# Kernel optimization log

Hardware: AMD Instinct MI355X
Metric: run time of the kernel (lower is better)

## Reference

```python
import jax, jax.numpy as jnp
import numpy as np

EPS = 1e-6
DIM_HEAD = 32
INP = 128
OUP = 128
IH = IW = 32


def _conv3x3(x, w):
    # NCHW conv, 3x3, stride 1, pad 1, no bias
    return jax.lax.conv_general_dilated(
        x, w, window_strides=(1, 1), padding=((1, 1), (1, 1)),
        dimension_numbers=("NCHW", "OIHW", "NCHW"))


def _groupnorm1(x, gamma, beta):
    # GroupNorm with 1 group: normalize over (C,H,W) per sample
    m = jnp.mean(x, axis=(1, 2, 3), keepdims=True)
    v = jnp.var(x, axis=(1, 2, 3), keepdims=True)
    xn = (x - m) * jax.lax.rsqrt(v + EPS)
    return xn * gamma[None, :, None, None] + beta[None, :, None, None]


def _proj(x, w, gamma, beta):
    return jax.nn.gelu(_groupnorm1(_conv3x3(x, w), gamma, beta), approximate=False)


def _relative_index(ih, iw):
    coords = np.stack(np.meshgrid(np.arange(ih), np.arange(iw), indexing="ij"))
    coords = coords.reshape(2, -1)  # (2, N)
    rel = coords[:, :, None] - coords[:, None, :]  # (2, N, N)
    rel[0] += ih - 1
    rel[1] += iw - 1
    rel[0] *= 2 * iw - 1
    return rel.sum(0).reshape(-1).astype(np.int32)  # (N*N,)


def setup_inputs() -> dict:
    key = jax.random.key(0)
    ks = jax.random.split(key, 12)
    B = 16
    x = jax.random.normal(ks[0], (B, INP, IH, IW), jnp.float32)
    w_scale = 0.05
    wq = jax.random.normal(ks[1], (INP, INP, 3, 3), jnp.float32) * w_scale
    wk = jax.random.normal(ks[2], (INP, INP, 3, 3), jnp.float32) * w_scale
    wv = jax.random.normal(ks[3], (INP, INP, 3, 3), jnp.float32) * w_scale
    gq = jnp.ones((INP,), jnp.float32); bq = jnp.zeros((INP,), jnp.float32)
    gk = jnp.ones((INP,), jnp.float32); bk = jnp.zeros((INP,), jnp.float32)
    gv = jnp.ones((INP,), jnp.float32); bv = jnp.zeros((INP,), jnp.float32)
    heads = INP // DIM_HEAD
    table = jax.random.normal(ks[4], ((2 * IH - 1) * (2 * IW - 1), heads), jnp.float32) * 0.02
    rel_index = jnp.asarray(_relative_index(IH, IW))
    out_w = jax.random.normal(ks[5], (OUP, INP, 1, 1), jnp.float32) * w_scale
    out_b = jnp.zeros((OUP,), jnp.float32)
    return {"x": x, "wq": wq, "gq": gq, "bq": bq, "wk": wk, "gk": gk, "bk": bk,
            "wv": wv, "gv": gv, "bv": bv, "table": table, "rel_index": rel_index,
            "out_w": out_w, "out_b": out_b}


def reference(x, wq, gq, bq, wk, gk, bk, wv, gv, bv, table, rel_index, out_w, out_b):
    B, C, ih, iw = x.shape
    H = C // DIM_HEAD
    N = ih * iw

    def to_heads(t):
        # b c ih iw -> b (ihiw) c -> b h n d (heads-major channel split)
        return t.reshape(B, C, N).transpose(0, 2, 1).reshape(B, N, H, DIM_HEAD).transpose(0, 2, 1, 3)

    q = to_heads(_proj(x, wq, gq, bq))
    k = to_heads(_proj(x, wk, gk, bk))
    v = to_heads(_proj(x, wv, gv, bv))

    # NOTE: original applies self.scale only when y is not None; y=None here -> no scale
    dots = jnp.einsum("bhnd,bhmd->bhnm", q, k)  # (B,H,N,N)

    bias = table[rel_index]                 # (N*N, H)
    bias = bias.reshape(N, N, H).transpose(2, 0, 1)[None]  # (1,H,N,N)
    attn = jax.nn.softmax(dots + bias, axis=-1)

    out = jnp.einsum("bhnm,bhmd->bhnd", attn, v)
    out = out.transpose(0, 2, 1, 3).reshape(B, N, C).transpose(0, 2, 1).reshape(B, C, ih, iw)
    # to_out: 1x1 conv + bias (Dropout2d is identity in eval)
    out = jax.lax.conv_general_dilated(
        out, out_w, window_strides=(1, 1), padding=((0, 0), (0, 0)),
        dimension_numbers=("NCHW", "OIHW", "NCHW")) + out_b[None, :, None, None]
    return out
```

## Files before the change

### kernel.cpp

```cpp
#include <hip/hip_runtime.h>

typedef unsigned short u16;
typedef unsigned int   u32;

#define NB   16
#define NC   128
#define NPIX 1024
#define NH   4
#define DH   32

typedef __attribute__((ext_vector_type(8))) short short8;
typedef __attribute__((ext_vector_type(4))) float f32x4;
typedef __attribute__((ext_vector_type(8))) _Float16 half8;

#define XROWS 1152

__device__ __forceinline__ float bf2f(u16 u) {
    return __uint_as_float(((u32)u) << 16);
}
__device__ __forceinline__ u16 f2bf(float f) {
    u32 u = __float_as_uint(f);
    u32 r = (u + 0x7fffu + ((u >> 16) & 1u)) >> 16;
    return (u16)r;
}
__device__ __forceinline__ u16 f2h(float f) {
    _Float16 h = (_Float16)f;
    u16 r; __builtin_memcpy(&r, &h, 2); return r;
}
__device__ __forceinline__ int pk_h2(float a, float b) {
    auto h = __builtin_amdgcn_cvt_pkrtz(a, b);
    int r; __builtin_memcpy(&r, &h, 4); return r;
}
__device__ __forceinline__ float loadf(const void* p, int i, int isf) {
    return isf ? ((const float*)p)[i] : bf2f(((const u16*)p)[i]);
}
__device__ __forceinline__ float4 load4(const void* p, int i4, int isf) {
    if (isf) return ((const float4*)p)[i4];
    ushort4 u = ((const ushort4*)p)[i4];
    return make_float4(bf2f(u.x), bf2f(u.y), bf2f(u.z), bf2f(u.w));
}
__device__ __forceinline__ int detect_isf(const void* x) {
    const u16* p = (const u16*)x;
    u16 v = p[threadIdx.x & 63];
    int e = (v >> 7) & 0xFF;
    unsigned long long m = __ballot(e >= 134);
    return m != 0ull ? 1 : 0;
}

__global__ __launch_bounds__(256) void prep_all(
        const void* __restrict__ x,
        const void* __restrict__ w0, const void* __restrict__ w1,
        const void* __restrict__ w2, const void* __restrict__ ow,
        const int* __restrict__ rel, const void* __restrict__ table,
        u16* __restrict__ Wt, u16* __restrict__ Wf, u16* __restrict__ xTp,
        u16* __restrict__ biasT, float* __restrict__ stats) {
    __shared__ __align__(16) u32 smem_u[4160];
    int isf = detect_isf(x);
    int bid = blockIdx.x;
    int t = threadIdx.x;

    if (bid < 1792) {
        if (bid == 0 && t < 96) stats[t] = 0.f;
        int i = bid * 256 + t;
        if (i < 442368) {
            int j   = i / 147456;
            int rr  = i % 147456;
            int tap = rr >> 14;
            int co  = (rr >> 7) & 127;
            int ci  = rr & 127;
            const void* w = (j == 0) ? w0 : ((j == 1) ? w1 : w2);
            float v = loadf(w, (co * 128 + ci) * 9 + tap, isf);
            int coh = (co >> 6) & 1, wm = (co >> 5) & 1;
            int mt  = (co >> 4) & 1, l16 = co & 15;
            int ks  = (ci >> 5) & 3, q  = (ci >> 3) & 3, e = ci & 7;
            int dst = (j * 9 + tap) * 16384
                    + (coh * 2 + wm) * 4096 + ks * 1024 + mt * 512
                    + (q * 16 + l16) * 8 + e;
            Wt[dst] = f2bf(v);
        } else {
            int i2 = i - 442368;
            if (i2 < 16384) {
                int co = i2 >> 7, k = i2 & 127;
                int zc = (co >> 6) & 1, wm = (co >> 5) & 1;
                int mt = (co >> 4) & 1, l16 = co & 15;
                int ks = (k >> 5) & 3, q = (k >> 3) & 3, e = k & 7;
                int dst = (zc * 2 + wm) * 4096 + ks * 1024 + mt * 512
                        + (q * 16 + l16) * 8 + e;
                Wf[dst] = f2h(loadf(ow, i2, isf));
            }
        }
    } else if (bid < 2304) {
        float* tile = (float*)smem_u;
        int b2 = bid - 1792;
        int pixg = b2 & 7, cig = (b2 >> 3) & 3, b = b2 >> 5;

        if (pixg == 0 || pixg == 7) {
            int row = (pixg == 0 ? 0 : 1088) + (t >> 2);
            int seg = t & 3;
            size_t dst = ((size_t)(b * XROWS + row)) * 128 + cig * 32 + seg * 8;
            *(uint4*)&xTp[dst] = make_uint4(0, 0, 0, 0);
        }

        int ci = t >> 3, px0 = (t & 7) * 16;
        int base = b * (NC * NPIX) + (cig * 32 + ci) * NPIX + pixg * 128 + px0;
#pragma unroll
        for (int u = 0; u < 4; ++u) {
            float4 v = load4(x, (base >> 2) + u, isf);
            float* d = &tile[ci * 129 + px0 + u * 4];
            d[0] = v.x; d[1] = v.y; d[2] = v.z; d[3] = v.w;
        }
        __syncthreads();
#pragma unroll
        for (int u = 0; u < 2; ++u) {
            int c = t + u * 256;
            int pix = c >> 2, seg = c & 3;
            u16 tmp[8];
#pragma unroll
            for (int e = 0; e < 8; ++e)
                tmp[e] = f2bf(tile[(seg * 8 + e) * 129 + pix]);
            size_t dst = ((size_t)(b * XROWS + 64 + pixg * 128 + pix)) * 128
                       + cig * 32 + seg * 8;
            *(ushort4*)&xTp[dst] =
                make_ushort4(tmp[0], tmp[1], tmp[2], tmp[3]);
            *(ushort4*)&xTp[dst + 4] =
                make_ushort4(tmp[4], tmp[5], tmp[6], tmp[7]);
        }
    } else {
        int* rl = (int*)smem_u;
        int b2 = bid - 2304;
        int nt = b2 & 15, mt = b2 >> 4;

#pragma unroll
        for (int c = 0; c < 16; ++c) {
            int i = t + c * 256;
            int r = i >> 6, cc = i & 63;
            rl[r * 65 + cc] = rel[(size_t)(nt * 64 + r) * 1024 + mt * 64 + cc];
        }
        __syncthreads();

#pragma unroll
        for (int h = 0; h < NH; ++h) {
#pragma unroll
            for (int c = 0; c < 16; ++c) {
                int wdx = t + c * 256;
                int r     = wdx & 3;
                int lane  = (wdx >> 2) & 63;
                int fragl = wdx >> 8;
                int n16l  = fragl >> 2;
                int m16l  = fragl & 3;
                int n_loc = n16l * 16 + (lane & 15);
                int m_loc = m16l * 16 + ((lane >> 4) << 2) + r;
                int ri = rl[n_loc * 65 + m_loc];
                float v = loadf(table, ri * NH + h, isf);
                biasT[((size_t)h << 20)
                      + ((size_t)((nt * 4 + n16l) * 64 + (mt * 4 + m16l)) << 8)
                      + lane * 4 + r] = f2bf(v);
            }
        }
    }
}

__global__ __launch_bounds__(256) void conv6_kernel(
        const u16* __restrict__ xTp, const u16* __restrict__ Wt,
        float* __restrict__ conv_out, float* __restrict__ stats) {
    __shared__ __align__(16) u16 Xh[194 * 128];

    int t = threadIdx.x;
    int bx = blockIdx.x, b = blockIdx.y, j = blockIdx.z;
    int pt = bx >> 1, coh = bx & 1;
    int p0 = pt * 128;
    int w = t >> 6, lane = t & 63;
    int q = lane >> 4, l16 = lane & 15;
    int cobase = coh * 64 + (w & 1) * 32;
    int pixbase = (w >> 1) * 64;

    const u16* xb  = xTp + ((size_t)b * XROWS + 64) * 128;
    const u16* wrb = Wt + (size_t)(j * 9) * 16384
                   + (coh * 2 + (w & 1)) * 4096 + lane * 8;

    short8 awA[2][4], awB[2][4];
#pragma unroll
    for (int ks = 0; ks < 4; ++ks) {
        awA[0][ks] = *(const short8*)(wrb + ks * 1024);
        awA[1][ks] = *(const short8*)(wrb + ks * 1024 + 512);
    }

#pragma unroll
    for (int k = 0; k < 13; ++k) {
        int c = t + k * 256;
        if (c < 194 * 16) {
            int row = c >> 4, seg = c & 15;
            int pg = p0 - 33 + row;
            uint4 v = *(const uint4*)(xb + (size_t)pg * 128 + seg * 8);
            *(uint4*)&Xh[row * 128 + ((seg + row) & 15) * 8] = v;
        }
    }
    __syncthreads();

    f32x4 acc[2][4];
#pragma unroll
    for (int mt = 0; mt < 2; ++mt)
#pragma unroll
        for (int nt = 0; nt < 4; ++nt) acc[mt][nt] = (f32x4)0.f;

#pragma unroll
    for (int tap = 0; tap < 9; ++tap) {
        const int dy = tap / 3, dx = tap % 3;
        bool inv_e = (dx == 0) && (l16 == 0);
        bool inv_o = (dx == 2) && (l16 == 15);
        int rbase = pixbase + dy * 32 + dx + l16;

        if (tap < 8) {
            const u16* nw = wrb + (size_t)(tap + 1) * 16384;
            if ((tap & 1) == 0) {
#pragma unroll
                for (int ks = 0; ks < 4; ++ks) {
                    awB[0][ks] = *(const short8*)(nw + ks * 1024);
                    awB[1][ks] = *(const short8*)(nw + ks * 1024 + 512);
                }
            } else {
#pragma unroll
                for (int ks = 0; ks < 4; ++ks) {
                    awA[0][ks] = *(const short8*)(nw + ks * 1024);
                    awA[1][ks] = *(const short8*)(nw + ks * 1024 + 512);
                }
            }
        }

#pragma unroll
        for (int ks = 0; ks < 4; ++ks) {
            int sl = ks * 4 + q;
            short8 bf[4];
#pragma unroll
            for (int nt = 0; nt < 4; ++nt) {
                int row = rbase + nt * 16;
                short8 v = *(const short8*)&Xh[row * 128
                                               + ((sl + row) & 15) * 8];
                bf[nt] = ((nt & 1) ? inv_o : inv_e) ? (short8)0 : v;
            }
#pragma unroll
            for (int mt = 0; mt < 2; ++mt) {
                short8 a = ((tap & 1) == 0) ? awA[mt][ks] : awB[mt][ks];
#pragma unroll
                for (int nt = 0; nt < 4; ++nt)
                    acc[mt][nt] = __builtin_amdgcn_mfma_f32_16x16x32_bf16(
                        a, bf[nt], acc[mt][nt], 0, 0, 0);
            }
        }
    }

    float s = 0.f, s2 = 0.f;
    size_t obase = ((size_t)(j * NB + b) * NC) * NPIX;
#pragma unroll
    for (int mt = 0; mt < 2; ++mt) {
#pragma unroll
        for (int nt = 0; nt < 4; ++nt) {
            f32x4 v = acc[mt][nt];
            int co  = cobase + mt * 16 + q * 4;
            int pix = p0 + pixbase + nt * 16 + l16;
#pragma unroll
            for (int r = 0; r < 4; ++r) {
                float val = v[r];
                conv_out[obase + (size_t)(co + r) * NPIX + pix] = val;
                s += val;
                s2 = fmaf(val, val, s2);
            }
        }
    }
#pragma unroll
    for (int off = 32; off; off >>= 1) {
        s  += __shfl_down(s,  (unsigned)off, 64);
        s2 += __shfl_down(s2, (unsigned)off, 64);
    }
    if (lane == 0) {
        atomicAdd(&stats[(j * NB + b) * 2 + 0], s);
        atomicAdd(&stats[(j * NB + b) * 2 + 1], s2);
    }
}

__global__ __launch_bounds__(256) void norm_kernel(
        const void* __restrict__ xdet,
        const float* __restrict__ conv_out, const float* __restrict__ stats,
        const void* __restrict__ g0, const void* __restrict__ b0,
        const void* __restrict__ g1, const void* __restrict__ b1,
        const void* __restrict__ g2, const void* __restrict__ b2,
        u16* __restrict__ qh, u16* __restrict__ kh, u16* __restrict__ vh) {
    __shared__ float tile[32 * 257];
    int isf = detect_isf(xdet);
    int t = threadIdx.x;
    int n0 = blockIdx.x * 256;
    int h = blockIdx.y;
    int z = blockIdx.z;
    int j = z >> 4;
    int b = z & 15;
    const void* gam = (j == 0) ? g0 : ((j == 1) ? g1 : g2);
    const void* bet = (j == 0) ? b0 : ((j == 1) ? b1 : b2);

    float sum = stats[z * 2], ss = stats[z * 2 + 1];
    const float inv = 1.0f / 131072.0f;
    float mean = sum * inv;
    float var  = fmaxf(ss * inv - mean * mean, 0.f);
    float rstd = rsqrtf(var + 1e-6f);

    const float* src = conv_out + ((size_t)z * NC + h * DH) * NPIX + n0;

    if (j == 2) {
        u16* dst = vh + (((size_t)(b * NH + h)) * DH) * NPIX + n0;
#pragma unroll
        for (int cl = 0; cl < 32; ++cl) {
            float v = src[cl * NPIX + t];
            v = (v - mean) * rstd * loadf(gam, h * DH + cl, isf)
              + loadf(bet, h * DH + cl, isf);
            v = 0.5f * v * (1.0f + erff(v * 0.70710678118654752f));
            dst[(size_t)cl * NPIX + t] = f2h(v);
        }
        return;
    }

#pragma unroll
    for (int cl = 0; cl < 32; ++cl) tile[cl * 257 + t] = src[cl * NPIX + t];
    __syncthreads();

    u16* dst = ((j == 0) ? qh : kh)
             + (((size_t)(b * NH + h)) * NPIX + n0) * DH;
#pragma unroll
    for (int k = 0; k < 32; ++k) {
        int o = t + k * 256;
        int d = o & 31, nl = o >> 5;
        float v = tile[d * 257 + nl];
        v = (v - mean) * rstd * loadf(gam, h * DH + d, isf)
          + loadf(bet, h * DH + d, isf);
        v = 0.5f * v * (1.0f + erff(v * 0.70710678118654752f));
        dst[o] = f2h(v);
    }
}

__global__ __launch_bounds__(256) void attn2_kernel(
        const u16* __restrict__ qh, const u16* __restrict__ kh,
        const u16* __restrict__ vh, const u16* __restrict__ biasT,
        u16* __restrict__ attfh) {
    int t = threadIdx.x;
    int b = blockIdx.x, h = blockIdx.y, qt = blockIdx.z;
    int w = t >> 6, lane = t & 63, q = lane >> 4, l16 = lane & 15;
    int nrow0 = qt * 128 + w * 32;

    const u16* qb = qh + (((size_t)(b * NH + h)) * NPIX) * DH;
    const u16* kb = kh + (((size_t)(b * NH + h)) * NPIX) * DH;
    const u16* vb = vh + (((size_t)(b * NH + h)) * DH) * NPIX;
    const u16* bf0 = biasT + ((size_t)h << 20)
                   + ((size_t)(qt * 8 + w * 2 + 0) << 14) + lane * 4;
    const u16* bf1 = biasT + ((size_t)h << 20)
                   + ((size_t)(qt * 8 + w * 2 + 1) << 14) + lane * 4;

    half8 qf[2];
#pragma unroll
    for (int nt = 0; nt < 2; ++nt)
        qf[nt] = *(const half8*)(qb + (size_t)(nrow0 + nt * 16 + l16) * DH
                                 + q * 8);

    f32x4 O[2][2];
#pragma unroll
    for (int dt = 0; dt < 2; ++dt)
#pragma unroll
        for (int nt = 0; nt < 2; ++nt) O[dt][nt] = (f32x4)0.f;
    float mrow[2] = {-1e30f, -1e30f}, lrow[2] = {0.f, 0.f};

    int addrLo = ((2 * (q & 1)) * 16 + l16) * 4;
    int addrHi = addrLo + 64;
    bool hiQ = (q >= 2);

    for (int kc = 0; kc < 8; ++kc) {
        int m0 = kc * 128;
        f32x4 St[8][2];
#pragma unroll
        for (int mt = 0; mt < 8; ++mt) {
            half8 kf = *(const half8*)(kb + (size_t)(m0 + mt * 16 + l16) * DH
                                       + q * 8);
            int m16 = kc * 8 + mt;
            ushort4 bv0 = *(const ushort4*)(bf0 + (m16 << 8));
            ushort4 bv1 = *(const ushort4*)(bf1 + (m16 << 8));
            f32x4 c0, c1;
            c0[0] = bf2f(bv0.x); c0[1] = bf2f(bv0.y);
            c0[2] = bf2f(bv0.z); c0[3] = bf2f(bv0.w);
            c1[0] = bf2f(bv1.x); c1[1] = bf2f(bv1.y);
            c1[2] = bf2f(bv1.z); c1[3] = bf2f(bv1.w);
            St[mt][0] = __builtin_amdgcn_mfma_f32_16x16x32_f16(
                kf, qf[0], c0, 0, 0, 0);
            St[mt][1] = __builtin_amdgcn_mfma_f32_16x16x32_f16(
                kf, qf[1], c1, 0, 0, 0);
        }
        float mx[2] = {-1e30f, -1e30f};
#pragma unroll
        for (int mt = 0; mt < 8; ++mt)
#pragma unroll
            for (int nt = 0; nt < 2; ++nt)
#pragma unroll
                for (int r = 0; r < 4; ++r)
                    mx[nt] = fmaxf(mx[nt], St[mt][nt][r]);
        float alpha[2];
#pragma unroll
        for (int nt = 0; nt < 2; ++nt) {
            mx[nt] = fmaxf(mx[nt], __shfl_xor(mx[nt], 16, 64));
            mx[nt] = fmaxf(mx[nt], __shfl_xor(mx[nt], 32, 64));
            float mn = fmaxf(mrow[nt], mx[nt]);
            alpha[nt] = __expf(mrow[nt] - mn);
            mrow[nt] = mn;
        }
        float sm[2] = {0.f, 0.f};
#pragma unroll
        for (int mt = 0; mt < 8; ++mt)
#pragma unroll
            for (int nt = 0; nt < 2; ++nt)
#pragma unroll
                for (int r = 0; r < 4; ++r) {
                    float p = __expf(St[mt][nt][r] - mrow[nt]);
                    St[mt][nt][r] = p;
                    sm[nt] += p;
                }
#pragma unroll
        for (int nt = 0; nt < 2; ++nt) {
            sm[nt] += __shfl_xor(sm[nt], 16, 64);
            sm[nt] += __shfl_xor(sm[nt], 32, 64);
            lrow[nt] = lrow[nt] * alpha[nt] + sm[nt];
        }
#pragma unroll
        for (int dt = 0; dt < 2; ++dt)
#pragma unroll
            for (int nt = 0; nt < 2; ++nt)
#pragma unroll
                for (int r = 0; r < 4; ++r)
                    O[dt][nt][r] *= alpha[nt];
#pragma unroll
        for (int ms = 0; ms < 4; ++ms) {
            half8 vf[2];
#pragma unroll
            for (int dt = 0; dt < 2; ++dt)
                vf[dt] = *(const half8*)(vb + (size_t)(dt * 16 + l16) * NPIX
                                         + m0 + ms * 32 + q * 8);
#pragma unroll
            for (int nt = 0; nt < 2; ++nt) {
                int p01_0 = pk_h2(St[2 * ms][nt][0],     St[2 * ms][nt][1]);
                int p23_0 = pk_h2(St[2 * ms][nt][2],     St[2 * ms][nt][3]);
                int p01_1 = pk_h2(St[2 * ms + 1][nt][0], St[2 * ms + 1][nt][1]);
                int p23_1 = pk_h2(St[2 * ms + 1][nt][2], St[2 * ms + 1][nt][3]);
                int a0 = __builtin_amdgcn_ds_bpermute(addrLo, p01_0);
                int a1 = __builtin_amdgcn_ds_bpermute(addrLo, p23_0);
                int a2 = __builtin_amdgcn_ds_bpermute(addrHi, p01_0);
                int a3 = __builtin_amdgcn_ds_bpermute(addrHi, p23_0);
                int b0 = __builtin_amdgcn_ds_bpermute(addrLo, p01_1);
                int b1 = __builtin_amdgcn_ds_bpermute(addrLo, p23_1);
                int b2 = __builtin_amdgcn_ds_bpermute(addrHi, p01_1);
                int b3 = __builtin_amdgcn_ds_bpermute(addrHi, p23_1);
                int pb[4];
                pb[0] = hiQ ? b0 : a0;
                pb[1] = hiQ ? b1 : a1;
                pb[2] = hiQ ? b2 : a2;
                pb[3] = hiQ ? b3 : a3;
                half8 pf; __builtin_memcpy(&pf, pb, 16);
#pragma unroll
                for (int dt = 0; dt < 2; ++dt)
                    O[dt][nt] = __builtin_amdgcn_mfma_f32_16x16x32_f16(
                        vf[dt], pf, O[dt][nt], 0, 0, 0);
            }
        }
    }

#pragma unroll
    for (int nt = 0; nt < 2; ++nt) {
        float rl = 1.0f / lrow[nt];
        int n = nrow0 + nt * 16 + l16;
        u16* dst = attfh + ((size_t)b * NPIX + n) * NC + h * DH;
#pragma unroll
        for (int dt = 0; dt < 2; ++dt) {
            f32x4 o = O[dt][nt];
            uint2 pv = make_uint2((u32)pk_h2(o[0] * rl, o[1] * rl),
                                  (u32)pk_h2(o[2] * rl, o[3] * rl));
            *(uint2*)(dst + dt * 16 + q * 4) = pv;
        }
    }
}

__global__ __launch_bounds__(256) void out3_kernel(
        const void* __restrict__ xdet,
        const u16* __restrict__ attfh, const u16* __restrict__ Wf,
        const void* __restrict__ ob, void* __restrict__ out) {
    int isf = detect_isf(xdet);
    int t = threadIdx.x;
    int n0 = blockIdx.x * 64, b = blockIdx.y, zc = blockIdx.z;
    int w = t >> 6, lane = t & 63, q = lane >> 4, l16 = lane & 15;
    int cobase = zc * 64 + (w & 1) * 32, nbase = (w >> 1) * 32;

    f32x4 acc[2][2];
#pragma unroll
    for (int mt = 0; mt < 2; ++mt)
#pragma unroll
        for (int nt = 0; nt < 2; ++nt) acc[mt][nt] = (f32x4)0.f;

    const u16* ab = attfh + ((size_t)b * NPIX + n0 + nbase) * NC;
    const u16* wfb = Wf + (zc * 2 + (w & 1)) * 4096 + lane * 8;
#pragma unroll
    for (int ks = 0; ks < 4; ++ks) {
        int k0 = ks * 32 + q * 8;
        half8 a[2], bfr[2];
#pragma unroll
        for (int mt = 0; mt < 2; ++mt)
            a[mt] = *(const half8*)(wfb + ks * 1024 + mt * 512);
#pragma unroll
        for (int nt = 0; nt < 2; ++nt)
            bfr[nt] = *(const half8*)(ab + (size_t)(nt * 16 + l16) * NC + k0);
#pragma unroll
        for (int mt = 0; mt < 2; ++mt)
#pragma unroll
            for (int nt = 0; nt < 2; ++nt)
                acc[mt][nt] = __builtin_amdgcn_mfma_f32_16x16x32_f16(
                    a[mt], bfr[nt], acc[mt][nt], 0, 0, 0);
    }

#pragma unroll
    for (int mt = 0; mt < 2; ++mt) {
#pragma unroll
        for (int nt = 0; nt < 2; ++nt) {
            f32x4 v = acc[mt][nt];
            int n = n0 + nbase + nt * 16 + l16;
#pragma unroll
            for (int r = 0; r < 4; ++r) {
                int co = cobase + mt * 16 + q * 4 + r;
                float val = v[r] + loadf(ob, co, isf);
                size_t oidx = ((size_t)b * NC + co) * NPIX + n;
                if (isf) ((float*)out)[oidx] = val;
                else     ((u16*)out)[oidx]   = f2bf(val);
            }
        }
    }
}

extern "C" void kernel_launch(void* const* d_in, const int* in_sizes, int n_in,
                              void* d_out, int out_size, void* d_ws,
                              size_t ws_size, hipStream_t stream) {
    (void)in_sizes; (void)n_in; (void)out_size; (void)ws_size;
    const void* x     = d_in[0];
    const void* wq    = d_in[1];
    const void* gq    = d_in[2];
    const void* bq    = d_in[3];
    const void* wk    = d_in[4];
    const void* gk    = d_in[5];
    const void* bk    = d_in[6];
    const void* wv    = d_in[7];
    const void* gv    = d_in[8];
    const void* bv    = d_in[9];
    const void* table = d_in[10];
    const int*  rel   = (const int*)d_in[11];
    const void* ow    = d_in[12];
    const void* ob    = d_in[13];

    char* ws = (char*)d_ws;
    float* stats = (float*)(ws);
    char*  regQ  = ws + 512;
    u16*   xTp   = (u16*)regQ;
    u16*   Wt    = (u16*)(regQ + 5242880);
    u16*   qhp   = (u16*)regQ;
    u16*   khp   = (u16*)(regQ + 4194304);
    u16*   vhp   = (u16*)(regQ + 8388608);
    u16*   biasT = (u16*)(regQ + 12582912);
    u16*   Wf    = (u16*)(regQ + 20971520);
    char*  regA  = regQ + 25165824;
    float* conv  = (float*)regA;
    u16*   attfh = (u16*)(regA + 8388608);

    prep_all<<<2560, 256, 0, stream>>>(x, wq, wk, wv, ow, rel, table,
                                       Wt, Wf, xTp, biasT, stats);
    conv6_kernel<<<dim3(16, 16, 3), 256, 0, stream>>>(xTp, Wt, conv, stats);
    norm_kernel<<<dim3(4, 4, 48), 256, 0, stream>>>(x, conv, stats,
                                                    gq, bq, gk, bk, gv, bv,
                                                    qhp, khp, vhp);
    attn2_kernel<<<dim3(16, 4, 8), 256, 0, stream>>>(qhp, khp, vhp, biasT,
                                                     attfh);
    out3_kernel<<<dim3(16, 16, 2), 256, 0, stream>>>(x, attfh, Wf, ob, d_out);
}
```

Before: 199.3 us.

## Halve per-wave query rows in attention to double grid size, skip unit rescale

```diff
diff --git a/kernel.cpp b/kernel.cpp
--- a/kernel.cpp
+++ b/kernel.cpp
@@ -342,28 +342,19 @@
     int t = threadIdx.x;
     int b = blockIdx.x, h = blockIdx.y, qt = blockIdx.z;
     int w = t >> 6, lane = t & 63, q = lane >> 4, l16 = lane & 15;
-    int nrow0 = qt * 128 + w * 32;
+    int nrow0 = qt * 64 + w * 16;
 
     const u16* qb = qh + (((size_t)(b * NH + h)) * NPIX) * DH;
     const u16* kb = kh + (((size_t)(b * NH + h)) * NPIX) * DH;
     const u16* vb = vh + (((size_t)(b * NH + h)) * DH) * NPIX;
     const u16* bf0 = biasT + ((size_t)h << 20)
-                   + ((size_t)(qt * 8 + w * 2 + 0) << 14) + lane * 4;
-    const u16* bf1 = biasT + ((size_t)h << 20)
-                   + ((size_t)(qt * 8 + w * 2 + 1) << 14) + lane * 4;
-
-    half8 qf[2];
-#pragma unroll
-    for (int nt = 0; nt < 2; ++nt)
-        qf[nt] = *(const half8*)(qb + (size_t)(nrow0 + nt * 16 + l16) * DH
-                                 + q * 8);
-
-    f32x4 O[2][2];
-#pragma unroll
-    for (int dt = 0; dt < 2; ++dt)
-#pragma unroll
-        for (int nt = 0; nt < 2; ++nt) O[dt][nt] = (f32x4)0.f;
-    float mrow[2] = {-1e30f, -1e30f}, lrow[2] = {0.f, 0.f};
+                   + ((size_t)(qt * 4 + w) << 14) + lane * 4;
+
+    half8 qf = *(const half8*)(qb + (size_t)(nrow0 + l16) * DH + q * 8);
+
+    f32x4 O[2];
+    O[0] = (f32x4)0.f; O[1] = (f32x4)0.f;
+    float mrow = -1e30f, lrow = 0.f;
 
     int addrLo = ((2 * (q & 1)) * 16 + l16) * 4;
     int addrHi = addrLo + 64;
@@ -371,65 +362,48 @@
 
     for (int kc = 0; kc < 8; ++kc) {
         int m0 = kc * 128;
-        f32x4 St[8][2];
+        f32x4 St[8];
 #pragma unroll
         for (int mt = 0; mt < 8; ++mt) {
             half8 kf = *(const half8*)(kb + (size_t)(m0 + mt * 16 + l16) * DH
                                        + q * 8);
-            int m16 = kc * 8 + mt;
-            ushort4 bv0 = *(const ushort4*)(bf0 + (m16 << 8));
-            ushort4 bv1 = *(const ushort4*)(bf1 + (m16 << 8));
-            f32x4 c0, c1;
-            c0[0] = bf2f(bv0.x); c0[1] = bf2f(bv0.y);
-            c0[2] = bf2f(bv0.z); c0[3] = bf2f(bv0.w);
-            c1[0] = bf2f(bv1.x); c1[1] = bf2f(bv1.y);
-            c1[2] = bf2f(bv1.z); c1[3] = bf2f(bv1.w);
-            St[mt][0] = __builtin_amdgcn_mfma_f32_16x16x32_f16(
-                kf, qf[0], c0, 0, 0, 0);
-            St[mt][1] = __builtin_amdgcn_mfma_f32_16x16x32_f16(
-                kf, qf[1], c1, 0, 0, 0);
-        }
-        float mx[2] = {-1e30f, -1e30f};
+            ushort4 bv = *(const ushort4*)(bf0 + ((kc * 8 + mt) << 8));
+            f32x4 c0;
+            c0[0] = bf2f(bv.x); c0[1] = bf2f(bv.y);
+            c0[2] = bf2f(bv.z); c0[3] = bf2f(bv.w);
+            St[mt] = __builtin_amdgcn_mfma_f32_16x16x32_f16(
+                kf, qf, c0, 0, 0, 0);
+        }
+        float mx = -1e30f;
 #pragma unroll
         for (int mt = 0; mt < 8; ++mt)
 #pragma unroll
-            for (int nt = 0; nt < 2; ++nt)
+            for (int r = 0; r < 4; ++r)
+                mx = fmaxf(mx, St[mt][r]);
+        mx = fmaxf(mx, __shfl_xor(mx, 16, 64));
+        mx = fmaxf(mx, __shfl_xor(mx, 32, 64));
+        float mn = fmaxf(mrow, mx);
+        float alpha = __expf(mrow - mn);
+        mrow = mn;
+        float sm = 0.f;
+#pragma unroll
+        for (int mt = 0; mt < 8; ++mt)
+#pragma unroll
+            for (int r = 0; r < 4; ++r) {
+                float p = __expf(St[mt][r] - mrow);
+                St[mt][r] = p;
+                sm += p;
+            }
+        sm += __shfl_xor(sm, 16, 64);
+        sm += __shfl_xor(sm, 32, 64);
+        lrow = lrow * alpha + sm;
+        if (!__all(alpha == 1.0f)) {
+#pragma unroll
+            for (int dt = 0; dt < 2; ++dt)
 #pragma unroll
                 for (int r = 0; r < 4; ++r)
-                    mx[nt] = fmaxf(mx[nt], St[mt][nt][r]);
-        float alpha[2];
-#pragma unroll
-        for (int nt = 0; nt < 2; ++nt) {
-            mx[nt] = fmaxf(mx[nt], __shfl_xor(mx[nt], 16, 64));
-            mx[nt] = fmaxf(mx[nt], __shfl_xor(mx[nt], 32, 64));
-            float mn = fmaxf(mrow[nt], mx[nt]);
-            alpha[nt] = __expf(mrow[nt] - mn);
-            mrow[nt] = mn;
-        }
-        float sm[2] = {0.f, 0.f};
-#pragma unroll
-        for (int mt = 0; mt < 8; ++mt)
-#pragma unroll
-            for (int nt = 0; nt < 2; ++nt)
-#pragma unroll
-                for (int r = 0; r < 4; ++r) {
-                    float p = __expf(St[mt][nt][r] - mrow[nt]);
-                    St[mt][nt][r] = p;
-                    sm[nt] += p;
-                }
-#pragma unroll
-        for (int nt = 0; nt < 2; ++nt) {
-            sm[nt] += __shfl_xor(sm[nt], 16, 64);
-            sm[nt] += __shfl_xor(sm[nt], 32, 64);
-            lrow[nt] = lrow[nt] * alpha[nt] + sm[nt];
-        }
-#pragma unroll
-        for (int dt = 0; dt < 2; ++dt)
-#pragma unroll
-            for (int nt = 0; nt < 2; ++nt)
-#pragma unroll
-                for (int r = 0; r < 4; ++r)
-                    O[dt][nt][r] *= alpha[nt];
+                    O[dt][r] *= alpha;
+        }
 #pragma unroll
         for (int ms = 0; ms < 4; ++ms) {
             half8 vf[2];
@@ -437,46 +411,40 @@
             for (int dt = 0; dt < 2; ++dt)
                 vf[dt] = *(const half8*)(vb + (size_t)(dt * 16 + l16) * NPIX
                                          + m0 + ms * 32 + q * 8);
-#pragma unroll
-            for (int nt = 0; nt < 2; ++nt) {
-                int p01_0 = pk_h2(St[2 * ms][nt][0],     St[2 * ms][nt][1]);
-                int p23_0 = pk_h2(St[2 * ms][nt][2],     St[2 * ms][nt][3]);
-                int p01_1 = pk_h2(St[2 * ms + 1][nt][0], St[2 * ms + 1][nt][1]);
-                int p23_1 = pk_h2(St[2 * ms + 1][nt][2], St[2 * ms + 1][nt][3]);
-                int a0 = __builtin_amdgcn_ds_bpermute(addrLo, p01_0);
-                int a1 = __builtin_amdgcn_ds_bpermute(addrLo, p23_0);
-                int a2 = __builtin_amdgcn_ds_bpermute(addrHi, p01_0);
-                int a3 = __builtin_amdgcn_ds_bpermute(addrHi, p23_0);
-                int b0 = __builtin_amdgcn_ds_bpermute(addrLo, p01_1);
-                int b1 = __builtin_amdgcn_ds_bpermute(addrLo, p23_1);
-                int b2 = __builtin_amdgcn_ds_bpermute(addrHi, p01_1);
-                int b3 = __builtin_amdgcn_ds_bpermute(addrHi, p23_1);
-                int pb[4];
-                pb[0] = hiQ ? b0 : a0;
-                pb[1] = hiQ ? b1 : a1;
-                pb[2] = hiQ ? b2 : a2;
-                pb[3] = hiQ ? b3 : a3;
-                half8 pf; __builtin_memcpy(&pf, pb, 16);
-#pragma unroll
-                for (int dt = 0; dt < 2; ++dt)
-                    O[dt][nt] = __builtin_amdgcn_mfma_f32_16x16x32_f16(
-                        vf[dt], pf, O[dt][nt], 0, 0, 0);
-            }
-        }
-    }
-
-#pragma unroll
-    for (int nt = 0; nt < 2; ++nt) {
-        float rl = 1.0f / lrow[nt];
-        int n = nrow0 + nt * 16 + l16;
-        u16* dst = attfh + ((size_t)b * NPIX + n) * NC + h * DH;
-#pragma unroll
-        for (int dt = 0; dt < 2; ++dt) {
-            f32x4 o = O[dt][nt];
-            uint2 pv = make_uint2((u32)pk_h2(o[0] * rl, o[1] * rl),
-                                  (u32)pk_h2(o[2] * rl, o[3] * rl));
-            *(uint2*)(dst + dt * 16 + q * 4) = pv;
-        }
+            int p01_0 = pk_h2(St[2 * ms][0],     St[2 * ms][1]);
+            int p23_0 = pk_h2(St[2 * ms][2],     St[2 * ms][3]);
+            int p01_1 = pk_h2(St[2 * ms + 1][0], St[2 * ms + 1][1]);
+            int p23_1 = pk_h2(St[2 * ms + 1][2], St[2 * ms + 1][3]);
+            int a0 = __builtin_amdgcn_ds_bpermute(addrLo, p01_0);
+            int a1 = __builtin_amdgcn_ds_bpermute(addrLo, p23_0);
+            int a2 = __builtin_amdgcn_ds_bpermute(addrHi, p01_0);
+            int a3 = __builtin_amdgcn_ds_bpermute(addrHi, p23_0);
+            int b0 = __builtin_amdgcn_ds_bpermute(addrLo, p01_1);
+            int b1 = __builtin_amdgcn_ds_bpermute(addrLo, p23_1);
+            int b2 = __builtin_amdgcn_ds_bpermute(addrHi, p01_1);
+            int b3 = __builtin_amdgcn_ds_bpermute(addrHi, p23_1);
+            int pb[4];
+            pb[0] = hiQ ? b0 : a0;
+            pb[1] = hiQ ? b1 : a1;
+            pb[2] = hiQ ? b2 : a2;
+            pb[3] = hiQ ? b3 : a3;
+            half8 pf; __builtin_memcpy(&pf, pb, 16);
+#pragma unroll
+            for (int dt = 0; dt < 2; ++dt)
+                O[dt] = __builtin_amdgcn_mfma_f32_16x16x32_f16(
+                    vf[dt], pf, O[dt], 0, 0, 0);
+        }
+    }
+
+    float rl = 1.0f / lrow;
+    int n = nrow0 + l16;
+    u16* dst = attfh + ((size_t)b * NPIX + n) * NC + h * DH;
+#pragma unroll
+    for (int dt = 0; dt < 2; ++dt) {
+        f32x4 o = O[dt];
+        uint2 pv = make_uint2((u32)pk_h2(o[0] * rl, o[1] * rl),
+                              (u32)pk_h2(o[2] * rl, o[3] * rl));
+        *(uint2*)(dst + dt * 16 + q * 4) = pv;
     }
 }
 
@@ -573,7 +541,7 @@
     norm_kernel<<<dim3(4, 4, 48), 256, 0, stream>>>(x, conv, stats,
                                                     gq, bq, gk, bk, gv, bv,
                                                     qhp, khp, vhp);
-    attn2_kernel<<<dim3(16, 4, 8), 256, 0, stream>>>(qhp, khp, vhp, biasT,
-                                                     attfh);
+    attn2_kernel<<<dim3(16, 4, 16), 256, 0, stream>>>(qhp, khp, vhp, biasT,
+                                                      attfh);
     out3_kernel<<<dim3(16, 16, 2), 256, 0, stream>>>(x, attfh, Wf, ob, d_out);
 }
```

New measurement: 227.4 us. 1.14x slower.

## Stage K/V tiles in double-buffered LDS and remap attention block order

Applied to the files above, without the earlier changes.

```diff
diff --git a/kernel.cpp b/kernel.cpp
--- a/kernel.cpp
+++ b/kernel.cpp
@@ -339,8 +339,15 @@
         const u16* __restrict__ qh, const u16* __restrict__ kh,
         const u16* __restrict__ vh, const u16* __restrict__ biasT,
         u16* __restrict__ attfh) {
+    __shared__ __align__(16) u16 Kl[2][128 * 40];
+    __shared__ __align__(16) u16 Vl[2][32 * 136];
+
     int t = threadIdx.x;
-    int b = blockIdx.x, h = blockIdx.y, qt = blockIdx.z;
+    int f = blockIdx.x;
+    int r_ = f >> 3;
+    int g = (f & 7) * 4 + (r_ >> 4);
+    int b = r_ & 15;
+    int h = g & 3, qt = g >> 2;
     int w = t >> 6, lane = t & 63, q = lane >> 4, l16 = lane & 15;
     int nrow0 = qt * 128 + w * 32;
 
@@ -352,6 +359,20 @@
     const u16* bf1 = biasT + ((size_t)h << 20)
                    + ((size_t)(qt * 8 + w * 2 + 1) << 14) + lane * 4;
 
+    int krow = t >> 2, kseg = t & 3;
+    int vrow = t >> 4, vseg = t & 15;
+
+    {
+        uint4 k0 = *(const uint4*)(kb + t * 8);
+        uint4 k1 = *(const uint4*)(kb + (t + 256) * 8);
+        uint4 v0 = *(const uint4*)(vb + vrow * NPIX + vseg * 8);
+        uint4 v1 = *(const uint4*)(vb + (vrow + 16) * NPIX + vseg * 8);
+        *(uint4*)&Kl[0][krow * 40 + kseg * 8] = k0;
+        *(uint4*)&Kl[0][(krow + 64) * 40 + kseg * 8] = k1;
+        *(uint4*)&Vl[0][vrow * 136 + vseg * 8] = v0;
+        *(uint4*)&Vl[0][(vrow + 16) * 136 + vseg * 8] = v1;
+    }
+
     half8 qf[2];
 #pragma unroll
     for (int nt = 0; nt < 2; ++nt)
@@ -369,13 +390,27 @@
     int addrHi = addrLo + 64;
     bool hiQ = (q >= 2);
 
+    __syncthreads();
+
     for (int kc = 0; kc < 8; ++kc) {
-        int m0 = kc * 128;
+        int cur = kc & 1;
+        const u16* Kc = &Kl[cur][0];
+        const u16* Vc = &Vl[cur][0];
+
+        uint4 pk0, pk1, pv0, pv1;
+        bool pf = (kc < 7);
+        if (pf) {
+            int m0n = (kc + 1) * 128;
+            pk0 = *(const uint4*)(kb + m0n * 32 + t * 8);
+            pk1 = *(const uint4*)(kb + m0n * 32 + (t + 256) * 8);
+            pv0 = *(const uint4*)(vb + vrow * NPIX + m0n + vseg * 8);
+            pv1 = *(const uint4*)(vb + (vrow + 16) * NPIX + m0n + vseg * 8);
+        }
+
         f32x4 St[8][2];
 #pragma unroll
         for (int mt = 0; mt < 8; ++mt) {
-            half8 kf = *(const half8*)(kb + (size_t)(m0 + mt * 16 + l16) * DH
-                                       + q * 8);
+            half8 kf = *(const half8*)&Kc[(mt * 16 + l16) * 40 + q * 8];
             int m16 = kc * 8 + mt;
             ushort4 bv0 = *(const ushort4*)(bf0 + (m16 << 8));
             ushort4 bv1 = *(const ushort4*)(bf1 + (m16 << 8));
@@ -423,20 +458,22 @@
             sm[nt] += __shfl_xor(sm[nt], 32, 64);
             lrow[nt] = lrow[nt] * alpha[nt] + sm[nt];
         }
-#pragma unroll
-        for (int dt = 0; dt < 2; ++dt)
-#pragma unroll
-            for (int nt = 0; nt < 2; ++nt)
-#pragma unroll
-                for (int r = 0; r < 4; ++r)
-                    O[dt][nt][r] *= alpha[nt];
+        if (!__all(alpha[0] == 1.0f && alpha[1] == 1.0f)) {
+#pragma unroll
+            for (int dt = 0; dt < 2; ++dt)
+#pragma unroll
+                for (int nt = 0; nt < 2; ++nt)
+#pragma unroll
+                    for (int r = 0; r < 4; ++r)
+                        O[dt][nt][r] *= alpha[nt];
+        }
 #pragma unroll
         for (int ms = 0; ms < 4; ++ms) {
             half8 vf[2];
 #pragma unroll
             for (int dt = 0; dt < 2; ++dt)
-                vf[dt] = *(const half8*)(vb + (size_t)(dt * 16 + l16) * NPIX
-                                         + m0 + ms * 32 + q * 8);
+                vf[dt] = *(const half8*)&Vc[(dt * 16 + l16) * 136
+                                            + ms * 32 + q * 8];
 #pragma unroll
             for (int nt = 0; nt < 2; ++nt) {
                 int p01_0 = pk_h2(St[2 * ms][nt][0],     St[2 * ms][nt][1]);
@@ -456,13 +493,20 @@
                 pb[1] = hiQ ? b1 : a1;
                 pb[2] = hiQ ? b2 : a2;
                 pb[3] = hiQ ? b3 : a3;
-                half8 pf; __builtin_memcpy(&pf, pb, 16);
+                half8 pf2; __builtin_memcpy(&pf2, pb, 16);
 #pragma unroll
                 for (int dt = 0; dt < 2; ++dt)
                     O[dt][nt] = __builtin_amdgcn_mfma_f32_16x16x32_f16(
-                        vf[dt], pf, O[dt][nt], 0, 0, 0);
-            }
-        }
+                        vf[dt], pf2, O[dt][nt], 0, 0, 0);
+            }
+        }
+        if (pf) {
+            *(uint4*)&Kl[cur ^ 1][krow * 40 + kseg * 8] = pk0;
+            *(uint4*)&Kl[cur ^ 1][(krow + 64) * 40 + kseg * 8] = pk1;
+            *(uint4*)&Vl[cur ^ 1][vrow * 136 + vseg * 8] = pv0;
+            *(uint4*)&Vl[cur ^ 1][(vrow + 16) * 136 + vseg * 8] = pv1;
+        }
+        __syncthreads();
     }
 
 #pragma unroll
@@ -573,7 +617,6 @@
     norm_kernel<<<dim3(4, 4, 48), 256, 0, stream>>>(x, conv, stats,
                                                     gq, bq, gk, bk, gv, bv,
                                                     qhp, khp, vhp);
-    attn2_kernel<<<dim3(16, 4, 8), 256, 0, stream>>>(qhp, khp, vhp, biasT,
-                                                     attfh);
+    attn2_kernel<<<512, 256, 0, stream>>>(qhp, khp, vhp, biasT, attfh);
     out3_kernel<<<dim3(16, 16, 2), 256, 0, stream>>>(x, attfh, Wf, ob, d_out);
 }
```

Measured after the change: 197.9 us. Within noise of the previous version (-0.7%).
